# Optimization experiments

Hardware: AMD Instinct MI355X
Metric: run time of the kernel (lower is better)

The kernel has to match this reference:

```python
import jax, jax.numpy as jnp
import numpy as np

D_K = 64
TAU = 1.0
THRESHOLD = 0.5


def setup_inputs() -> dict:
    key = jax.random.key(0)
    k1, k2, k3 = jax.random.split(key, 3)
    B, N, F = 32, 512, 320
    F_OBS = 256
    h = jax.random.normal(k1, (B, N, F), dtype=jnp.float32)
    # xavier_uniform with gain 1.414 on (F_OBS, D_K)
    limit = float(1.414 * np.sqrt(6.0 / (F_OBS + D_K)))
    a_link = jax.random.uniform(k2, (F_OBS, D_K), minval=-limit, maxval=limit, dtype=jnp.float32)
    b_link = jax.random.uniform(k3, (F_OBS, D_K), minval=-limit, maxval=limit, dtype=jnp.float32)
    return {"h": h, "a_link": a_link, "b_link": b_link, "rollout": 1}


def reference(h, a_link, b_link, rollout):
    F_OBS = a_link.shape[0]
    # original detaches the sliced features
    hx = jax.lax.stop_gradient(h[:, :, :F_OBS])
    h_i = jnp.einsum('bik,kl->bil', hx, a_link)
    h_j = jnp.einsum('bjk,kl->bjl', hx, b_link)
    logits = jnp.einsum('bil,bjl->bij', h_i, h_j) / jnp.sqrt(jnp.float32(D_K))

    # gumbel_sigmoid with rollout=True: no noise, just sigmoid(logits/tau)
    y_soft = jax.nn.sigmoid(logits / TAU)
    y_hard = (y_soft > THRESHOLD).astype(y_soft.dtype)
    # straight-through estimator
    A = y_hard - jax.lax.stop_gradient(y_soft) + y_soft

    B, N, _ = logits.shape
    eye_b = jnp.eye(N, dtype=bool)[None]          # [1, N, N]
    eye_f = jnp.eye(N, dtype=y_soft.dtype)[None]  # [1, N, N]

    # log-prob of the sampled hard edges, off-diagonal entries only
    sel = A * y_soft + (1.0 - A) * (1.0 - y_soft)
    logp = jnp.log(sel + 1e-8)
    probs = jnp.sum(jnp.where(eye_b, 0.0, logp), axis=(1, 2))  # [B]

    # zero the diagonal of A, then add identity (vectorized form of the per-batch diag loop)
    A_out = A - A * eye_f + eye_f
    # .squeeze(0) is a no-op for B > 1
    return A_out, probs
```

## Files before the change

kernel.cpp:

```cpp
#include <hip/hip_runtime.h>
#include <math.h>

#define BATCH   32
#define NPTS    512
#define FDIM    320
#define FOBS    256
#define DK      64
#define MROWS   (BATCH * NPTS)
#define A_ELEMS ((size_t)BATCH * NPTS * NPTS)

typedef __bf16  bf16x8 __attribute__((ext_vector_type(8)));
typedef float   f32x4  __attribute__((ext_vector_type(4)));
typedef ushort  u16x8  __attribute__((ext_vector_type(8)));

__device__ __forceinline__ ushort f2bf(float f) {
    unsigned u = __builtin_bit_cast(unsigned, f);
    return (ushort)((u + 0x7fffu + ((u >> 16) & 1u)) >> 16);
}

__device__ __forceinline__ bf16x8 ld_bf8(const ushort* p) {
    return __builtin_bit_cast(bf16x8, *reinterpret_cast<const uint4*>(p));
}

__global__ __launch_bounds__(256) void k0_wt(const float* __restrict__ al,
                                             const float* __restrict__ bl,
                                             ushort* __restrict__ wt) {
    const int n = blockIdx.x;
    const int k = threadIdx.x;
    const float* src = (n < 64) ? al : bl;
    const int nn = n & 63;
    wt[(size_t)n * FOBS + k] = f2bf(src[(size_t)k * DK + nn]);
}

__global__ __launch_bounds__(256) void k1_mfma(const float* __restrict__ h,
                                               const ushort* __restrict__ wt,
                                               ushort* __restrict__ hi,
                                               ushort* __restrict__ hj) {
    const int t  = threadIdx.x;
    const int w  = t >> 6;
    const int l  = t & 63;
    const int lr = l & 15;
    const int lg = l >> 4;
    const int rb = blockIdx.x * 32 + 16 * (w & 1);
    const int cb = 64 * (w >> 1);

    const float* hrow = h + (size_t)(rb + lr) * FDIM;
    bf16x8 afr[8];
#pragma unroll
    for (int ks = 0; ks < 8; ++ks) {
        const float* p = hrow + ks * 32 + lg * 8;
        float4 v0 = *reinterpret_cast<const float4*>(p);
        float4 v1 = *reinterpret_cast<const float4*>(p + 4);
        u16x8 u;
        u[0] = f2bf(v0.x); u[1] = f2bf(v0.y); u[2] = f2bf(v0.z); u[3] = f2bf(v0.w);
        u[4] = f2bf(v1.x); u[5] = f2bf(v1.y); u[6] = f2bf(v1.z); u[7] = f2bf(v1.w);
        afr[ks] = __builtin_bit_cast(bf16x8, u);
    }

    f32x4 acc[4];
#pragma unroll
    for (int cf = 0; cf < 4; ++cf) acc[cf] = (f32x4){0.f, 0.f, 0.f, 0.f};

#pragma unroll
    for (int ks = 0; ks < 8; ++ks) {
#pragma unroll
        for (int cf = 0; cf < 4; ++cf) {
            bf16x8 bfr = ld_bf8(&wt[(size_t)(cb + 16 * cf + lr) * FOBS + ks * 32 + lg * 8]);
            acc[cf] = __builtin_amdgcn_mfma_f32_16x16x32_bf16(afr[ks], bfr, acc[cf], 0, 0, 0);
        }
    }

    ushort* dst = (cb == 0) ? hi : hj;
#pragma unroll
    for (int cf = 0; cf < 4; ++cf) {
        const int nn = 16 * cf + lr;
#pragma unroll
        for (int r = 0; r < 4; ++r) {
            const int m = rb + lg * 4 + r;
            dst[(size_t)m * DK + nn] = f2bf(acc[cf][r]);
        }
    }
}

__global__ __launch_bounds__(256, 4) void k2_mfma(const ushort* __restrict__ hi,
                                                  const ushort* __restrict__ hj,
                                                  float* __restrict__ Aout,
                                                  float* __restrict__ partials) {
    __shared__ float red[4];
    const int id  = blockIdx.x;
    const int sub = id >> 3;
    const int b   = (id & 7) * 4 + (sub >> 6);
    const int it  = (sub >> 3) & 7;
    const int jt  = sub & 7;

    const int t  = threadIdx.x;
    const int w  = t >> 6;
    const int l  = t & 63;
    const int lr = l & 15;
    const int lg = l >> 4;
    const int i0 = it * 64, j0 = jt * 64;

    const ushort* hib = hi + ((size_t)b * NPTS + i0) * DK;
    const ushort* hjb = hj + ((size_t)b * NPTS + j0) * DK;

    bf16x8 afr[2];
#pragma unroll
    for (int ks = 0; ks < 2; ++ks)
        afr[ks] = ld_bf8(&hib[(size_t)(16 * w + lr) * DK + ks * 32 + lg * 8]);

    bf16x8 bfr[4][2];
#pragma unroll
    for (int jtt = 0; jtt < 4; ++jtt)
#pragma unroll
        for (int ks = 0; ks < 2; ++ks)
            bfr[jtt][ks] = ld_bf8(&hjb[(size_t)(16 * jtt + lr) * DK + ks * 32 + lg * 8]);

    f32x4 acc[4];
#pragma unroll
    for (int jtt = 0; jtt < 4; ++jtt) acc[jtt] = (f32x4){0.f, 0.f, 0.f, 0.f};

#pragma unroll
    for (int ks = 0; ks < 2; ++ks)
#pragma unroll
        for (int jtt = 0; jtt < 4; ++jtt)
            acc[jtt] = __builtin_amdgcn_mfma_f32_16x16x32_bf16(
                afr[ks], bfr[jtt][ks], acc[jtt], 0, 0, 0);

    float lsum = 0.f;
    const int drow0 = i0 + 16 * w + lg * 4;
#pragma unroll
    for (int jtt = 0; jtt < 4; ++jtt) {
        const int col = j0 + 16 * jtt + lr;
#pragma unroll
        for (int r = 0; r < 4; ++r) {
            const int row = drow0 + r;
            float x  = acc[jtt][r] * 0.125f;
            float ax = fabsf(x);
            float nl = __logf(1.0f + __expf(-ax));
            bool diag = (row == col);
            float ov = (diag || x > 0.f) ? 1.f : 0.f;
            if (!diag) lsum -= nl;
            __builtin_nontemporal_store(ov, &Aout[((size_t)b * NPTS + row) * NPTS + col]);
        }
    }

#pragma unroll
    for (int off = 32; off > 0; off >>= 1) lsum += __shfl_down(lsum, off);
    if (l == 0) red[w] = lsum;
    __syncthreads();
    if (t == 0) {
        float s = (red[0] + red[1]) + (red[2] + red[3]);
        partials[(size_t)b * 64 + it * 8 + jt] = s;
    }
}

__global__ __launch_bounds__(64) void k3_reduce(const float* __restrict__ partials,
                                                float* __restrict__ probs) {
    int b = blockIdx.x;
    float s = partials[(size_t)b * 64 + threadIdx.x];
#pragma unroll
    for (int off = 32; off > 0; off >>= 1) s += __shfl_down(s, off);
    if (threadIdx.x == 0) probs[b] = s;
}

extern "C" void kernel_launch(void* const* d_in, const int* in_sizes, int n_in,
                              void* d_out, int out_size, void* d_ws, size_t ws_size,
                              hipStream_t stream) {
    const float* h  = (const float*)d_in[0];
    const float* al = (const float*)d_in[1];
    const float* bl = (const float*)d_in[2];
    float* out = (float*)d_out;

    ushort* hi      = (ushort*)d_ws;
    ushort* hj      = hi + (size_t)MROWS * DK;
    ushort* wt      = hj + (size_t)MROWS * DK;
    float* partials = (float*)(wt + 128 * FOBS);

    k0_wt<<<128, 256, 0, stream>>>(al, bl, wt);

    k1_mfma<<<MROWS / 32, 256, 0, stream>>>(h, wt, hi, hj);

    k2_mfma<<<(NPTS / 64) * (NPTS / 64) * BATCH, 256, 0, stream>>>(hi, hj, out, partials);

    k3_reduce<<<BATCH, 64, 0, stream>>>(partials, out + A_ELEMS);
}
```

Measured before the change: 38.58 us.

## Swap MFMA operand roles for vectorized stores and fuse final reduction

Both MFMA kernels swap their A and B operands, so each lane's accumulator holds four consecutive columns of one row. The first kernel can then write hi/hj as 4-wide vectors, and the second can write A as 16-byte nontemporal float4 stores instead of scalar stores. The separate per-batch reduction kernel is removed: the last block of each batch, found with an atomic counter reset in k0, sums the partials. This cuts store instruction count and one kernel launch, at the cost of atomics, fences and a counter that must be reset on every call.

```diff
diff --git a/kernel.cpp b/kernel.cpp
--- a/kernel.cpp
+++ b/kernel.cpp
@@ -12,6 +12,7 @@
 typedef __bf16  bf16x8 __attribute__((ext_vector_type(8)));
 typedef float   f32x4  __attribute__((ext_vector_type(4)));
 typedef ushort  u16x8  __attribute__((ext_vector_type(8)));
+typedef ushort  u16x4  __attribute__((ext_vector_type(4)));
 
 __device__ __forceinline__ ushort f2bf(float f) {
     unsigned u = __builtin_bit_cast(unsigned, f);
@@ -24,9 +25,11 @@
 
 __global__ __launch_bounds__(256) void k0_wt(const float* __restrict__ al,
                                              const float* __restrict__ bl,
-                                             ushort* __restrict__ wt) {
+                                             ushort* __restrict__ wt,
+                                             unsigned* __restrict__ cnt) {
     const int n = blockIdx.x;
     const int k = threadIdx.x;
+    if (n == 0 && k < BATCH) cnt[k] = 0u;
     const float* src = (n < 64) ? al : bl;
     const int nn = n & 63;
     wt[(size_t)n * FOBS + k] = f2bf(src[(size_t)k * DK + nn]);
@@ -45,7 +48,7 @@
     const int cb = 64 * (w >> 1);
 
     const float* hrow = h + (size_t)(rb + lr) * FDIM;
-    bf16x8 afr[8];
+    bf16x8 bfr[8];
 #pragma unroll
     for (int ks = 0; ks < 8; ++ks) {
         const float* p = hrow + ks * 32 + lg * 8;
@@ -54,7 +57,7 @@
         u16x8 u;
         u[0] = f2bf(v0.x); u[1] = f2bf(v0.y); u[2] = f2bf(v0.z); u[3] = f2bf(v0.w);
         u[4] = f2bf(v1.x); u[5] = f2bf(v1.y); u[6] = f2bf(v1.z); u[7] = f2bf(v1.w);
-        afr[ks] = __builtin_bit_cast(bf16x8, u);
+        bfr[ks] = __builtin_bit_cast(bf16x8, u);
     }
 
     f32x4 acc[4];
@@ -65,28 +68,30 @@
     for (int ks = 0; ks < 8; ++ks) {
 #pragma unroll
         for (int cf = 0; cf < 4; ++cf) {
-            bf16x8 bfr = ld_bf8(&wt[(size_t)(cb + 16 * cf + lr) * FOBS + ks * 32 + lg * 8]);
-            acc[cf] = __builtin_amdgcn_mfma_f32_16x16x32_bf16(afr[ks], bfr, acc[cf], 0, 0, 0);
+            bf16x8 afr = ld_bf8(&wt[(size_t)(cb + 16 * cf + lr) * FOBS + ks * 32 + lg * 8]);
+            acc[cf] = __builtin_amdgcn_mfma_f32_16x16x32_bf16(afr, bfr[ks], acc[cf], 0, 0, 0);
         }
     }
 
     ushort* dst = (cb == 0) ? hi : hj;
+    const size_t m = (size_t)(rb + lr);
 #pragma unroll
     for (int cf = 0; cf < 4; ++cf) {
-        const int nn = 16 * cf + lr;
+        u16x4 v;
 #pragma unroll
-        for (int r = 0; r < 4; ++r) {
-            const int m = rb + lg * 4 + r;
-            dst[(size_t)m * DK + nn] = f2bf(acc[cf][r]);
-        }
+        for (int r = 0; r < 4; ++r) v[r] = f2bf(acc[cf][r]);
+        *reinterpret_cast<u16x4*>(&dst[m * DK + 16 * cf + lg * 4]) = v;
     }
 }
 
 __global__ __launch_bounds__(256, 4) void k2_mfma(const ushort* __restrict__ hi,
                                                   const ushort* __restrict__ hj,
                                                   float* __restrict__ Aout,
-                                                  float* __restrict__ partials) {
+                                                  float* __restrict__ partials,
+                                                  unsigned* __restrict__ cnt,
+                                                  float* __restrict__ probs) {
     __shared__ float red[4];
+    __shared__ int   is_last;
     const int id  = blockIdx.x;
     const int sub = id >> 3;
     const int b   = (id & 7) * 4 + (sub >> 6);
@@ -106,42 +111,43 @@
     bf16x8 afr[2];
 #pragma unroll
     for (int ks = 0; ks < 2; ++ks)
-        afr[ks] = ld_bf8(&hib[(size_t)(16 * w + lr) * DK + ks * 32 + lg * 8]);
+        afr[ks] = ld_bf8(&hjb[(size_t)(16 * w + lr) * DK + ks * 32 + lg * 8]);
 
     bf16x8 bfr[4][2];
 #pragma unroll
-    for (int jtt = 0; jtt < 4; ++jtt)
+    for (int itt = 0; itt < 4; ++itt)
 #pragma unroll
         for (int ks = 0; ks < 2; ++ks)
-            bfr[jtt][ks] = ld_bf8(&hjb[(size_t)(16 * jtt + lr) * DK + ks * 32 + lg * 8]);
+            bfr[itt][ks] = ld_bf8(&hib[(size_t)(16 * itt + lr) * DK + ks * 32 + lg * 8]);
 
     f32x4 acc[4];
 #pragma unroll
-    for (int jtt = 0; jtt < 4; ++jtt) acc[jtt] = (f32x4){0.f, 0.f, 0.f, 0.f};
+    for (int itt = 0; itt < 4; ++itt) acc[itt] = (f32x4){0.f, 0.f, 0.f, 0.f};
 
 #pragma unroll
     for (int ks = 0; ks < 2; ++ks)
 #pragma unroll
-        for (int jtt = 0; jtt < 4; ++jtt)
-            acc[jtt] = __builtin_amdgcn_mfma_f32_16x16x32_bf16(
-                afr[ks], bfr[jtt][ks], acc[jtt], 0, 0, 0);
+        for (int itt = 0; itt < 4; ++itt)
+            acc[itt] = __builtin_amdgcn_mfma_f32_16x16x32_bf16(
+                afr[ks], bfr[itt][ks], acc[itt], 0, 0, 0);
 
     float lsum = 0.f;
-    const int drow0 = i0 + 16 * w + lg * 4;
+    const int colbase = j0 + 16 * w + lg * 4;
 #pragma unroll
-    for (int jtt = 0; jtt < 4; ++jtt) {
-        const int col = j0 + 16 * jtt + lr;
+    for (int itt = 0; itt < 4; ++itt) {
+        const int row = i0 + 16 * itt + lr;
+        f32x4 ov;
 #pragma unroll
         for (int r = 0; r < 4; ++r) {
-            const int row = drow0 + r;
-            float x  = acc[jtt][r] * 0.125f;
+            float x  = acc[itt][r] * 0.125f;
             float ax = fabsf(x);
             float nl = __logf(1.0f + __expf(-ax));
-            bool diag = (row == col);
-            float ov = (diag || x > 0.f) ? 1.f : 0.f;
+            bool diag = (row == colbase + r);
+            ov[r] = (diag || x > 0.f) ? 1.f : 0.f;
             if (!diag) lsum -= nl;
-            __builtin_nontemporal_store(ov, &Aout[((size_t)b * NPTS + row) * NPTS + col]);
         }
+        __builtin_nontemporal_store(ov,
+            reinterpret_cast<f32x4*>(&Aout[((size_t)b * NPTS + row) * NPTS + colbase]));
     }
 
 #pragma unroll
@@ -151,16 +157,20 @@
     if (t == 0) {
         float s = (red[0] + red[1]) + (red[2] + red[3]);
         partials[(size_t)b * 64 + it * 8 + jt] = s;
+        __threadfence();
+        unsigned old = atomicAdd(&cnt[b], 1u);
+        is_last = (old == 63u) ? 1 : 0;
     }
-}
+    __syncthreads();
 
-__global__ __launch_bounds__(64) void k3_reduce(const float* __restrict__ partials,
-                                                float* __restrict__ probs) {
-    int b = blockIdx.x;
-    float s = partials[(size_t)b * 64 + threadIdx.x];
+    if (is_last && t < 64) {
+        __threadfence();
+        const volatile float* pp = partials + (size_t)b * 64;
+        float s = pp[t];
 #pragma unroll
-    for (int off = 32; off > 0; off >>= 1) s += __shfl_down(s, off);
-    if (threadIdx.x == 0) probs[b] = s;
+        for (int off = 32; off > 0; off >>= 1) s += __shfl_down(s, off);
+        if (t == 0) probs[b] = s;
+    }
 }
 
 extern "C" void kernel_launch(void* const* d_in, const int* in_sizes, int n_in,
@@ -175,12 +185,12 @@
     ushort* hj      = hi + (size_t)MROWS * DK;
     ushort* wt      = hj + (size_t)MROWS * DK;
     float* partials = (float*)(wt + 128 * FOBS);
+    unsigned* cnt   = (unsigned*)(partials + BATCH * 64);
 
-    k0_wt<<<128, 256, 0, stream>>>(al, bl, wt);
+    k0_wt<<<128, 256, 0, stream>>>(al, bl, wt, cnt);
 
     k1_mfma<<<MROWS / 32, 256, 0, stream>>>(h, wt, hi, hj);
 
-    k2_mfma<<<(NPTS / 64) * (NPTS / 64) * BATCH, 256, 0, stream>>>(hi, hj, out, partials);
-
-    k3_reduce<<<BATCH, 64, 0, stream>>>(partials, out + A_ELEMS);
+    k2_mfma<<<(NPTS / 64) * (NPTS / 64) * BATCH, 256, 0, stream>>>(
+        hi, hj, out, partials, cnt, out + A_ELEMS);
 }
```

New measurement: 109.4 us. 2.84x slower.
